# Kernel optimization log

Measured on AMD Instinct MI355X. Metric: run time of the kernel, lower is better.

The kernel has to match this reference:

```python
import jax, jax.numpy as jnp
import numpy as np

B, S, T = 256, 1024, 64

def setup_inputs() -> dict:
    key = jax.random.key(0)
    k1, k2, k3, k4, k5 = jax.random.split(key, 5)
    emissions = jax.random.normal(k1, (B, S, T), dtype=jnp.float32)
    tags = jax.random.randint(k2, (B, S), 0, T, dtype=jnp.int64)
    mask = jnp.ones((B, S), dtype=jnp.int32)
    transitions = jax.random.normal(k3, (T, T), dtype=jnp.float32) * 0.1
    start_transitions = jax.random.normal(k4, (T,), dtype=jnp.float32) * 0.1
    end_transitions = jax.random.normal(k5, (T,), dtype=jnp.float32) * 0.1
    return {"emissions": emissions, "tags": tags, "mask": mask,
            "transitions": transitions, "start_transitions": start_transitions,
            "end_transitions": end_transitions}


def _gold_score(emissions, tags, maskf, transitions, start_transitions, end_transitions):
    # emission score at each gold tag: [B, S]
    emit = jnp.take_along_axis(emissions, tags[:, :, None], axis=2)[:, :, 0]
    # transition score between consecutive gold tags: [B, S-1]
    trans = transitions[tags[:, :-1], tags[:, 1:]]
    score = start_transitions[tags[:, 0]] + emit[:, 0]
    score = score + jnp.sum((trans + emit[:, 1:]) * maskf[:, 1:], axis=1)
    last_pos = maskf.astype(jnp.int32).sum(axis=1) - 1           # [B]
    last_tags = jnp.take_along_axis(tags, last_pos[:, None], axis=1)[:, 0]
    return score + end_transitions[last_tags]


def _log_partition(emissions, maskf, transitions, start_transitions, end_transitions):
    alpha0 = start_transitions[None, :] + emissions[:, 0]        # [B, T]

    def step(alpha, xs):
        emit_t, m_t = xs                                         # [B, T], [B]
        # scores[b, i, j] = alpha[b, i] + transitions[i, j] + emit_t[b, j]
        scores = alpha[:, :, None] + transitions[None, :, :] + emit_t[:, None, :]
        new_alpha = jax.nn.logsumexp(scores, axis=1)             # [B, T]
        alpha = jnp.where(m_t[:, None] > 0, new_alpha, alpha)
        return alpha, None

    xs = (jnp.swapaxes(emissions[:, 1:], 0, 1), jnp.swapaxes(maskf[:, 1:], 0, 1))
    alpha, _ = jax.lax.scan(step, alpha0, xs)
    return jax.nn.logsumexp(alpha + end_transitions[None, :], axis=1)  # [B]


def reference(emissions, tags, mask, transitions, start_transitions, end_transitions):
    maskf = mask.astype(emissions.dtype)
    log_Z = _log_partition(emissions, maskf, transitions, start_transitions, end_transitions)
    score = _gold_score(emissions, tags, maskf, transitions, start_transitions, end_transitions)
    return jnp.mean(log_Z - score)
```

## Files before the change

### kernel.cpp

```cpp
#include <hip/hip_runtime.h>

#define Bn 256
#define Sn 1024
#define Tn 64
#define NCH 16
#define BURN 64
#define SLAB 4
#define RAWSTR 260
#define CROW 72
#define MROW 129
#define LN2 0.69314718055994531f
#define L7LN2 4.8520302639196169f

typedef __attribute__((ext_vector_type(8))) short short8;
typedef __attribute__((ext_vector_type(4))) float f32x4;

__device__ __forceinline__ unsigned short f2bf_rne(float f) {
  unsigned u = __float_as_uint(f);
  u = (u + 0x7fffu + ((u >> 16) & 1u)) >> 16;
  return (unsigned short)u;
}
__device__ __forceinline__ unsigned pk2(float hi, float lo) {
  return __builtin_amdgcn_perm(__float_as_uint(hi), __float_as_uint(lo), 0x07060302);
}
__device__ __forceinline__ unsigned pke(float a, float b) {
  return (unsigned)f2bf_rne(__expf(a - L7LN2)) |
         ((unsigned)f2bf_rne(__expf(b - L7LN2)) << 16);
}
__device__ __forceinline__ void gl_lds16(const void* src, void* dst) {
  __builtin_amdgcn_global_load_lds(
      (const __attribute__((address_space(1))) void*)src,
      (__attribute__((address_space(3))) void*)dst, 16, 0, 0);
}
__device__ __forceinline__ void gl_lds4(const void* src, void* dst) {
  __builtin_amdgcn_global_load_lds(
      (const __attribute__((address_space(1))) void*)src,
      (__attribute__((address_space(3))) void*)dst, 4, 0, 0);
}

__global__ __launch_bounds__(128, 1) void crf_scan(
    const float* __restrict__ em, const int* __restrict__ tags,
    const int* __restrict__ mask, const float* __restrict__ trans,
    const float* __restrict__ startt, const float* __restrict__ endt,
    float* __restrict__ wsL, float* __restrict__ wsGold,
    int* __restrict__ wsM, float* __restrict__ wsSE, float* __restrict__ wsA,
    int* __restrict__ cnt, float* __restrict__ out) {
  const int g = blockIdx.x & 15;
  const int c = blockIdx.x >> 4;
  const int Wc = (c == 0) ? 0 : BURN;
  const int Lc = (c == NCH - 1) ? 63 : 64;
  const int TOT = Wc + Lc;
  const int NSLAB = (TOT + SLAB - 1) / SLAB;
  const int t0 = 64 * c + 1;
  const int tstart = t0 - Wc;
  const int tid = threadIdx.x;
  const int wid = tid >> 6;
  const int lane = tid & 63;
  const int m = lane & 15;
  const int q = lane >> 4;

  __shared__ __align__(16) float rawS[2][16 * RAWSTR];
  __shared__ __align__(16) short convS[2][SLAB * 16 * CROW];
  __shared__ __align__(16) short alpha[16 * CROW];
  __shared__ int maskL[16 * MROW];
  __shared__ int lastF;
  __shared__ float eend[64];
  __shared__ float rsum[2];

  short8 a00, a01, a10, a11, a20, a21, a30, a31;
  uint2 st0, st1, st2, st3;
  float Slog = 0.f;
  int K = 0, NL = 0;
  const f32x4 zero4 = {0.f, 0.f, 0.f, 0.f};

  auto issue_slab = [&](int s) {
    if (s >= NSLAB) return;
    float* dstb = rawS[s & 1];
    const int rem = TOT - 4 * s;
    if (rem >= SLAB) {
      for (int mm = 0; mm < 16; ++mm)
        gl_lds16(em + ((size_t)(16 * g + mm) * Sn + tstart + 4 * s) * 64 + lane * 4,
                 dstb + mm * RAWSTR);
    } else {
      for (int mm = 0; mm < 16; ++mm)
        for (int u = 0; u < rem; ++u)
          gl_lds4(em + ((size_t)(16 * g + mm) * Sn + tstart + 4 * s + u) * 64 + lane,
                  dstb + mm * RAWSTR + u * 64);
    }
  };
  auto convert_slab = [&](int s) {
    if (s >= NSLAB) return;
    const int mm = lane & 15, seg = lane >> 4;
    const float* rp = rawS[s & 1] + mm * RAWSTR + seg * 16;
    short* cb = convS[s & 1];
    const int vu = min(SLAB, TOT - 4 * s);
    for (int u = 0; u < vu; ++u) {
      float4 v0 = *(const float4*)(rp + u * 64 + 0);
      float4 v1 = *(const float4*)(rp + u * 64 + 4);
      float4 v2 = *(const float4*)(rp + u * 64 + 8);
      float4 v3 = *(const float4*)(rp + u * 64 + 12);
      uint4 w0, w1;
      w0.x = pke(v0.x, v0.y); w0.y = pke(v0.z, v0.w);
      w0.z = pke(v1.x, v1.y); w0.w = pke(v1.z, v1.w);
      w1.x = pke(v2.x, v2.y); w1.y = pke(v2.z, v2.w);
      w1.z = pke(v3.x, v3.y); w1.w = pke(v3.z, v3.w);
      short* cw = cb + (u * 16 + mm) * CROW + seg * 16;
      *(uint4*)(cw) = w0;
      *(uint4*)(cw + 8) = w1;
    }
  };

  if (wid == 0) {
#define LOADA(tm, kc, dst) { \
    _Pragma("unroll") for (int jj = 0; jj < 8; ++jj) { \
      int kk = kc * 32 + q * 8 + jj; \
      dst[jj] = (short)f2bf_rne(__expf(trans[kk * Tn + 16 * tm + m])); \
    } }
    LOADA(0, 0, a00) LOADA(0, 1, a01) LOADA(1, 0, a10) LOADA(1, 1, a11)
    LOADA(2, 0, a20) LOADA(2, 1, a21) LOADA(3, 0, a30) LOADA(3, 1, a31)
#undef LOADA
    if (c == 0) {
#define INIT0(tm, ss) { \
      float4 sv = *(const float4*)(startt + 16 * tm + 4 * q); \
      float4 ev = *(const float4*)(em + (size_t)(16 * g + m) * Sn * Tn + 16 * tm + 4 * q); \
      ss.x = (unsigned)f2bf_rne(__expf(sv.x + ev.x)) | \
             ((unsigned)f2bf_rne(__expf(sv.y + ev.y)) << 16); \
      ss.y = (unsigned)f2bf_rne(__expf(sv.z + ev.z)) | \
             ((unsigned)f2bf_rne(__expf(sv.w + ev.w)) << 16); }
      INIT0(0, st0) INIT0(1, st1) INIT0(2, st2) INIT0(3, st3)
#undef INIT0
    } else {
      st0.x = 0x3F803F80u; st0.y = 0x3F803F80u; st1 = st0; st2 = st0; st3 = st0;
    }
    issue_slab(0);
  } else {
    for (int mm = 0; mm < 16; ++mm) {
      gl_lds4(mask + (size_t)(16 * g + mm) * Sn + tstart + lane,
              (void*)(maskL + mm * MROW));
      bool special = (c == NCH - 1) && (g == 15) && (mm == 15);
      if (!special)
        gl_lds4(mask + (size_t)(16 * g + mm) * Sn + tstart + 64 + lane,
                (void*)(maskL + mm * MROW + 64));
    }
    {
      const int bm = 16 * g + m;
      const int qq = q;
      const int* tg = tags + (size_t)bm * Sn;
      const int* mkb = mask + (size_t)bm * Sn;
      const float* emb = em + (size_t)bm * Sn * Tn;
      float acc = 0.f;
      int cntg = 0;
      #pragma unroll 4
      for (int i = 0; i < 16; ++i) {
        int t = t0 + qq + 4 * i;
        bool ok = t < t0 + Lc;
        int ts = ok ? t : t0;
        int mv = mkb[ts];
        int tp = tg[ts - 1], tc = tg[ts];
        float w = trans[tp * Tn + tc] + emb[(size_t)ts * Tn + tc];
        acc += (ok && mv) ? w : 0.f;
        cntg += ok ? mv : 0;
      }
      acc += __shfl_xor(acc, 16); acc += __shfl_xor(acc, 32);
      cntg += __shfl_xor(cntg, 16); cntg += __shfl_xor(cntg, 32);
      if (qq == 0) { wsGold[c * 256 + bm] = acc; wsM[c * 256 + bm] = cntg; }
    }
    if (c == NCH - 1 && g == 15) {
      int t = tstart + 64 + lane;
      if (t < Sn) maskL[15 * MROW + 64 + lane] = mask[(size_t)255 * Sn + t];
    }
  }
  asm volatile("s_waitcnt vmcnt(0)" ::: "memory");
  __syncthreads();

  if (wid == 0) issue_slab(1);
  else convert_slab(0);
  asm volatile("s_waitcnt vmcnt(0)" ::: "memory");
  __syncthreads();

#define UNP(ss, x0, x1, x2, x3) \
  x0 = __uint_as_float(ss.x << 16); x1 = __uint_as_float(ss.x & 0xffff0000u); \
  x2 = __uint_as_float(ss.y << 16); x3 = __uint_as_float(ss.y & 0xffff0000u);

  for (int r = 0; r < NSLAB; ++r) {
    if (wid == 0) {
      issue_slab(r + 2);
      const short* cbase = convS[r & 1];
      short* arow = alpha + m * CROW;
      #pragma unroll
      for (int u = 0; u < SLAB; ++u) {
        const int tt = 4 * r + u;
        if (tt < TOT) {
          if (((r & 1) == 0) && u == 0) {
            float x00, x01, x02, x03, x10, x11, x12, x13;
            float x20, x21, x22, x23, x30, x31, x32, x33;
            UNP(st0, x00, x01, x02, x03) UNP(st1, x10, x11, x12, x13)
            UNP(st2, x20, x21, x22, x23) UNP(st3, x30, x31, x32, x33)
            float sm = (((x00 + x01) + (x02 + x03)) + ((x10 + x11) + (x12 + x13)))
                     + (((x20 + x21) + (x22 + x23)) + ((x30 + x31) + (x32 + x33)));
            sm += __shfl_xor(sm, 16); sm += __shfl_xor(sm, 32);
            if (c != 0 && tt == BURN) { Slog = __logf(sm); K = 0; NL = 0; }
            int k = 127 - (int)((__float_as_uint(sm) >> 23) & 255u);
            float fk = __uint_as_float((unsigned)(127 + k) << 23);
            x00 *= fk; x01 *= fk; x02 *= fk; x03 *= fk;
            x10 *= fk; x11 *= fk; x12 *= fk; x13 *= fk;
            x20 *= fk; x21 *= fk; x22 *= fk; x23 *= fk;
            x30 *= fk; x31 *= fk; x32 *= fk; x33 *= fk;
            st0.x = pk2(x01, x00); st0.y = pk2(x03, x02);
            st1.x = pk2(x11, x10); st1.y = pk2(x13, x12);
            st2.x = pk2(x21, x20); st2.y = pk2(x23, x22);
            st3.x = pk2(x31, x30); st3.y = pk2(x33, x32);
            K += k;
          }
          const short* ep = cbase + (u * 16 + m) * CROW;
          uint2 eu0 = *(const uint2*)(ep + 0 + 4 * q);
          uint2 eu1 = *(const uint2*)(ep + 16 + 4 * q);
          uint2 eu2 = *(const uint2*)(ep + 32 + 4 * q);
          uint2 eu3 = *(const uint2*)(ep + 48 + 4 * q);
          int mv = maskL[m * MROW + tt];
          *(uint2*)(arow + 4 * q) = st0;
          *(uint2*)(arow + 16 + 4 * q) = st1;
          *(uint2*)(arow + 32 + 4 * q) = st2;
          *(uint2*)(arow + 48 + 4 * q) = st3;
          short8 b0 = *(const short8*)(arow + q * 8);
          short8 b1 = *(const short8*)(arow + 32 + q * 8);
          f32x4 d0 = __builtin_amdgcn_mfma_f32_16x16x32_bf16(a00, b0, zero4, 0, 0, 0);
          f32x4 d1 = __builtin_amdgcn_mfma_f32_16x16x32_bf16(a10, b0, zero4, 0, 0, 0);
          f32x4 d2 = __builtin_amdgcn_mfma_f32_16x16x32_bf16(a20, b0, zero4, 0, 0, 0);
          f32x4 d3 = __builtin_amdgcn_mfma_f32_16x16x32_bf16(a30, b0, zero4, 0, 0, 0);
          d0 = __builtin_amdgcn_mfma_f32_16x16x32_bf16(a01, b1, d0, 0, 0, 0);
          d1 = __builtin_amdgcn_mfma_f32_16x16x32_bf16(a11, b1, d1, 0, 0, 0);
          d2 = __builtin_amdgcn_mfma_f32_16x16x32_bf16(a21, b1, d2, 0, 0, 0);
          d3 = __builtin_amdgcn_mfma_f32_16x16x32_bf16(a31, b1, d3, 0, 0, 0);
          const bool live = (mv != 0);
#define EPI(dd, eu, ss) { \
          float e0 = __uint_as_float(eu.x << 16); \
          float e1 = __uint_as_float(eu.x & 0xffff0000u); \
          float e2 = __uint_as_float(eu.y << 16); \
          float e3 = __uint_as_float(eu.y & 0xffff0000u); \
          unsigned nx = pk2(dd[1] * e1, dd[0] * e0); \
          unsigned ny = pk2(dd[3] * e3, dd[2] * e2); \
          ss.x = live ? nx : ss.x; \
          ss.y = live ? ny : ss.y; }
          EPI(d0, eu0, st0) EPI(d1, eu1, st1) EPI(d2, eu2, st2) EPI(d3, eu3, st3)
#undef EPI
          NL += (live && tt >= Wc) ? 1 : 0;
        }
      }
    } else {
      convert_slab(r + 1);
    }
    asm volatile("s_waitcnt vmcnt(0)" ::: "memory");
    __syncthreads();
  }

  if (wid == 0) {
    float x00, x01, x02, x03, x10, x11, x12, x13;
    float x20, x21, x22, x23, x30, x31, x32, x33;
    UNP(st0, x00, x01, x02, x03) UNP(st1, x10, x11, x12, x13)
    UNP(st2, x20, x21, x22, x23) UNP(st3, x30, x31, x32, x33)
    float sm = (((x00 + x01) + (x02 + x03)) + ((x10 + x11) + (x12 + x13)))
             + (((x20 + x21) + (x22 + x23)) + ((x30 + x31) + (x32 + x33)));
    sm += __shfl_xor(sm, 16); sm += __shfl_xor(sm, 32);
    const int bm = 16 * g + m;
    float L = __logf(sm) - Slog + LN2 * (float)(7 * NL - K);
    if (q == 0) wsL[c * 256 + bm] = L;
    if (c == NCH - 1) {
      if (q == 0) wsSE[bm] = __logf(sm);
      wsA[(0 + 4 * q + 0) * 256 + bm] = x00;  wsA[(0 + 4 * q + 1) * 256 + bm] = x01;
      wsA[(0 + 4 * q + 2) * 256 + bm] = x02;  wsA[(0 + 4 * q + 3) * 256 + bm] = x03;
      wsA[(16 + 4 * q + 0) * 256 + bm] = x10; wsA[(16 + 4 * q + 1) * 256 + bm] = x11;
      wsA[(16 + 4 * q + 2) * 256 + bm] = x12; wsA[(16 + 4 * q + 3) * 256 + bm] = x13;
      wsA[(32 + 4 * q + 0) * 256 + bm] = x20; wsA[(32 + 4 * q + 1) * 256 + bm] = x21;
      wsA[(32 + 4 * q + 2) * 256 + bm] = x22; wsA[(32 + 4 * q + 3) * 256 + bm] = x23;
      wsA[(48 + 4 * q + 0) * 256 + bm] = x30; wsA[(48 + 4 * q + 1) * 256 + bm] = x31;
      wsA[(48 + 4 * q + 2) * 256 + bm] = x32; wsA[(48 + 4 * q + 3) * 256 + bm] = x33;
    }
  }
#undef UNP

  __threadfence();
  __syncthreads();
  if (tid == 0) lastF = (atomicAdd(cnt, 1) == 255) ? 1 : 0;
  __syncthreads();
  if (lastF) {
    __threadfence();
    if (tid < 64) eend[tid] = __expf(endt[tid]);
    __syncthreads();
    float vsum = 0.f;
    for (int bb = tid; bb < Bn; bb += 128) {
      float sumL = 0.f, gold = 0.f;
      int msum = 0;
      #pragma unroll
      for (int cc = 0; cc < NCH; ++cc) {
        sumL += wsL[cc * 256 + bb];
        gold += wsGold[cc * 256 + bb];
        msum += wsM[cc * 256 + bb];
      }
      msum += mask[(size_t)bb * Sn];
      float se = 0.f;
      for (int jj = 0; jj < Tn; ++jj) se += wsA[jj * 256 + bb] * eend[jj];
      float logZ = sumL + __logf(se) - wsSE[bb];
      int tg0 = tags[(size_t)bb * Sn];
      int lastTag = tags[(size_t)bb * Sn + (msum - 1)];
      gold += startt[tg0] + em[(size_t)bb * Sn * Tn + tg0] + endt[lastTag];
      vsum += logZ - gold;
    }
    #pragma unroll
    for (int o = 32; o > 0; o >>= 1) vsum += __shfl_xor(vsum, o, 64);
    if (lane == 0) rsum[wid] = vsum;
    __syncthreads();
    if (tid == 0) out[0] = (rsum[0] + rsum[1]) * (1.0f / Bn);
  }
}

extern "C" void kernel_launch(void* const* d_in, const int* in_sizes, int n_in,
                              void* d_out, int out_size, void* d_ws, size_t ws_size,
                              hipStream_t stream) {
  const float* em     = (const float*)d_in[0];
  const int*   tags   = (const int*)d_in[1];
  const int*   mask   = (const int*)d_in[2];
  const float* trans  = (const float*)d_in[3];
  const float* startt = (const float*)d_in[4];
  const float* endt   = (const float*)d_in[5];
  float* out = (float*)d_out;

  float* wsL    = (float*)d_ws;
  float* wsGold = wsL + NCH * 256;
  int*   wsM    = (int*)(wsGold + NCH * 256);
  float* wsSE   = (float*)(wsM + NCH * 256);
  float* wsA    = wsSE + 256;
  int*   cnt    = (int*)(wsA + 64 * 256);

  hipMemsetAsync(cnt, 0, sizeof(int), stream);
  crf_scan<<<256, 128, 0, stream>>>(em, tags, mask, trans, startt, endt,
                                    wsL, wsGold, wsM, wsSE, wsA, cnt, out);
}
```

Baseline: 172.4 us.

## Deepen raw emission prefetch ring to five slabs with partial vmcnt barriers

Grows the raw LDS staging buffer from double to five-deep, so wave 0 keeps up to four slabs of emission loads in flight. It replaces the full vmcnt(0) wait before each barrier with partial waits (vmcnt 48/32/16) that cover only the slab about to be converted. It also issues the first slab before the transition-matrix setup and unrolls the gold-score and final dot loops further. The aim is to hide global-load latency behind the serial MFMA recurrence, at the cost of more LDS use (lower occupancy) and fragile hand-written vmcnt counting that assumes 16 loads per slab.

```diff
diff --git a/kernel.cpp b/kernel.cpp
--- a/kernel.cpp
+++ b/kernel.cpp
@@ -6,6 +6,7 @@
 #define NCH 16
 #define BURN 64
 #define SLAB 4
+#define RAWD 5
 #define RAWSTR 260
 #define CROW 72
 #define MROW 129
@@ -14,6 +15,11 @@
 
 typedef __attribute__((ext_vector_type(8))) short short8;
 typedef __attribute__((ext_vector_type(4))) float f32x4;
+
+#define BAR_W0_V48() asm volatile("s_waitcnt vmcnt(48) lgkmcnt(0)\n\ts_barrier" ::: "memory")
+#define BAR_W0_V32() asm volatile("s_waitcnt vmcnt(32) lgkmcnt(0)\n\ts_barrier" ::: "memory")
+#define BAR_W0_V16() asm volatile("s_waitcnt vmcnt(16) lgkmcnt(0)\n\ts_barrier" ::: "memory")
+#define BAR_FULL()   asm volatile("s_waitcnt vmcnt(0) lgkmcnt(0)\n\ts_barrier" ::: "memory")
 
 __device__ __forceinline__ unsigned short f2bf_rne(float f) {
   unsigned u = __float_as_uint(f);
@@ -59,7 +65,7 @@
   const int m = lane & 15;
   const int q = lane >> 4;
 
-  __shared__ __align__(16) float rawS[2][16 * RAWSTR];
+  __shared__ __align__(16) float rawS[RAWD][16 * RAWSTR];
   __shared__ __align__(16) short convS[2][SLAB * 16 * CROW];
   __shared__ __align__(16) short alpha[16 * CROW];
   __shared__ int maskL[16 * MROW];
@@ -75,7 +81,7 @@
 
   auto issue_slab = [&](int s) {
     if (s >= NSLAB) return;
-    float* dstb = rawS[s & 1];
+    float* dstb = rawS[s % RAWD];
     const int rem = TOT - 4 * s;
     if (rem >= SLAB) {
       for (int mm = 0; mm < 16; ++mm)
@@ -91,7 +97,7 @@
   auto convert_slab = [&](int s) {
     if (s >= NSLAB) return;
     const int mm = lane & 15, seg = lane >> 4;
-    const float* rp = rawS[s & 1] + mm * RAWSTR + seg * 16;
+    const float* rp = rawS[s % RAWD] + mm * RAWSTR + seg * 16;
     short* cb = convS[s & 1];
     const int vu = min(SLAB, TOT - 4 * s);
     for (int u = 0; u < vu; ++u) {
@@ -111,6 +117,7 @@
   };
 
   if (wid == 0) {
+    issue_slab(0);
 #define LOADA(tm, kc, dst) { \
     _Pragma("unroll") for (int jj = 0; jj < 8; ++jj) { \
       int kk = kc * 32 + q * 8 + jj; \
@@ -132,7 +139,6 @@
     } else {
       st0.x = 0x3F803F80u; st0.y = 0x3F803F80u; st1 = st0; st2 = st0; st3 = st0;
     }
-    issue_slab(0);
   } else {
     for (int mm = 0; mm < 16; ++mm) {
       gl_lds4(mask + (size_t)(16 * g + mm) * Sn + tstart + lane,
@@ -144,15 +150,14 @@
     }
     {
       const int bm = 16 * g + m;
-      const int qq = q;
       const int* tg = tags + (size_t)bm * Sn;
       const int* mkb = mask + (size_t)bm * Sn;
       const float* emb = em + (size_t)bm * Sn * Tn;
       float acc = 0.f;
       int cntg = 0;
-      #pragma unroll 4
+      #pragma unroll 16
       for (int i = 0; i < 16; ++i) {
-        int t = t0 + qq + 4 * i;
+        int t = t0 + q + 4 * i;
         bool ok = t < t0 + Lc;
         int ts = ok ? t : t0;
         int mv = mkb[ts];
@@ -163,20 +168,22 @@
       }
       acc += __shfl_xor(acc, 16); acc += __shfl_xor(acc, 32);
       cntg += __shfl_xor(cntg, 16); cntg += __shfl_xor(cntg, 32);
-      if (qq == 0) { wsGold[c * 256 + bm] = acc; wsM[c * 256 + bm] = cntg; }
+      if (q == 0) { wsGold[c * 256 + bm] = acc; wsM[c * 256 + bm] = cntg; }
     }
     if (c == NCH - 1 && g == 15) {
       int t = tstart + 64 + lane;
       if (t < Sn) maskL[15 * MROW + 64 + lane] = mask[(size_t)255 * Sn + t];
     }
   }
-  asm volatile("s_waitcnt vmcnt(0)" ::: "memory");
-  __syncthreads();
-
-  if (wid == 0) issue_slab(1);
-  else convert_slab(0);
-  asm volatile("s_waitcnt vmcnt(0)" ::: "memory");
-  __syncthreads();
+  BAR_FULL();
+
+  if (wid == 0) {
+    issue_slab(1); issue_slab(2); issue_slab(3); issue_slab(4);
+    BAR_W0_V48();
+  } else {
+    convert_slab(0);
+    BAR_FULL();
+  }
 
 #define UNP(ss, x0, x1, x2, x3) \
   x0 = __uint_as_float(ss.x << 16); x1 = __uint_as_float(ss.x & 0xffff0000u); \
@@ -184,7 +191,7 @@
 
   for (int r = 0; r < NSLAB; ++r) {
     if (wid == 0) {
-      issue_slab(r + 2);
+      issue_slab(r + 5);
       const short* cbase = convS[r & 1];
       short* arow = alpha + m * CROW;
       #pragma unroll
@@ -247,11 +254,14 @@
           NL += (live && tt >= Wc) ? 1 : 0;
         }
       }
+      if (r + 5 < NSLAB)      { BAR_W0_V48(); }
+      else if (r + 4 < NSLAB) { BAR_W0_V32(); }
+      else if (r + 3 < NSLAB) { BAR_W0_V16(); }
+      else                    { BAR_FULL(); }
     } else {
       convert_slab(r + 1);
-    }
-    asm volatile("s_waitcnt vmcnt(0)" ::: "memory");
-    __syncthreads();
+      BAR_FULL();
+    }
   }
 
   if (wid == 0) {
@@ -299,6 +309,7 @@
       }
       msum += mask[(size_t)bb * Sn];
       float se = 0.f;
+      #pragma unroll 8
       for (int jj = 0; jj < Tn; ++jj) se += wsA[jj * 256 + bb] * eend[jj];
       float logZ = sumL + __logf(se) - wsSE[bb];
       int tg0 = tags[(size_t)bb * Sn];
```

Measured after the change: 173.3 us. No clear change (+0.5%).
